# Performance work log

Hardware: AMD Instinct MI355X
Metric: run time of the kernel (lower is better)

## Reference

```python
import jax, jax.numpy as jnp
import numpy as np

B, T, C = 64, 1024, 32   # batch, seq_len, n_embd
H, D = 4, 8              # num_heads, head_size (H*D == C)


def setup_inputs() -> dict:
    key = jax.random.key(0)
    ks = jax.random.split(key, 6)
    s = 0.02  # init scale for weights
    x = jax.random.normal(ks[0], (B, T, C), dtype=jnp.float32)
    Wq = jax.random.normal(ks[1], (H, C, D), dtype=jnp.float32) * s
    Wk = jax.random.normal(ks[2], (H, C, D), dtype=jnp.float32) * s
    Wv = jax.random.normal(ks[3], (H, C, D), dtype=jnp.float32) * s
    Wproj = jax.random.normal(ks[4], (H * D, C), dtype=jnp.float32) * s
    bproj = jnp.zeros((C,), dtype=jnp.float32)
    return {"x": x, "Wq": Wq, "Wk": Wk, "Wv": Wv, "Wproj": Wproj, "bproj": bproj}


def reference(x, Wq, Wk, Wv, Wproj, bproj):
    # All heads batched into one einsum instead of a Python loop over Head modules.
    q = jnp.einsum('btc,hcd->bhtd', x, Wq)
    k = jnp.einsum('btc,hcd->bhtd', x, Wk)
    v = jnp.einsum('btc,hcd->bhtd', x, Wv)
    scale = D ** -0.5
    att = jnp.einsum('bhtd,bhsd->bhts', q, k) * scale  # [B,H,T,T]
    causal = jnp.tril(jnp.ones((T, T), dtype=bool))
    att = jnp.where(causal, att, jnp.float32(-1e9))
    att = jax.nn.softmax(att, axis=-1)  # dropout omitted (eval mode)
    o = jnp.einsum('bhts,bhsd->bhtd', att, v)
    o = o.transpose(0, 2, 1, 3).reshape(B, T, H * D)  # concat heads on last dim
    return o @ Wproj + bproj  # final proj; output dropout omitted (eval mode)
```

## Files before the change

### kernel.cpp

```cpp
#include <hip/hip_runtime.h>
#include <math.h>

static constexpr int Bb = 64, Tt = 1024, Cc = 32, Hh = 4, Dd = 8;
static constexpr float QSCALE = 0.51006973f;

typedef _Float16 h2  __attribute__((ext_vector_type(2)));
typedef _Float16 v4h __attribute__((ext_vector_type(4)));
typedef float  f32x4 __attribute__((ext_vector_type(4)));

__device__ __forceinline__ h2 pkrtz(float a, float b) {
  return __builtin_bit_cast(h2, __builtin_amdgcn_cvt_pkrtz(a, b));
}

__device__ __forceinline__ float fdot2(h2 a, h2 b, float c) {
#if __has_builtin(__builtin_amdgcn_fdot2)
  return __builtin_amdgcn_fdot2(a, b, c, false);
#else
  return fmaf((float)a.x, (float)b.x, fmaf((float)a.y, (float)b.y, c));
#endif
}

__device__ __forceinline__ float frcp(float x) {
#if __has_builtin(__builtin_amdgcn_rcpf)
  return __builtin_amdgcn_rcpf(x);
#else
  return 1.0f / x;
#endif
}

__device__ __forceinline__ float bperm_f32(int src_lane, float v) {
  return __builtin_bit_cast(float,
      __builtin_amdgcn_ds_bpermute(src_lane << 2, __builtin_bit_cast(int, v)));
}

__device__ __forceinline__ h2 exp2h2(h2 s) {
  const h2 A3 = {(_Float16)0.05550411f, (_Float16)0.05550411f};
  const h2 A2 = {(_Float16)0.24022651f, (_Float16)0.24022651f};
  const h2 A1 = {(_Float16)0.69314718f, (_Float16)0.69314718f};
  const h2 ONE = {(_Float16)1.0f, (_Float16)1.0f};
  h2 t = A3 * s + A2;
  t = t * s + A1;
  t = t * s + ONE;
  return t;
}

union U4 { uint4 u; h2 h[4]; };
union P2 { uint2 u; h2 h[2]; v4h v; };

__device__ __forceinline__ void chain_step(const P2& ak, const v4h& bv,
                                           const P2& bq, f32x4& o) {
  const f32x4 zero4 = {0.f, 0.f, 0.f, 0.f};
  f32x4 s = __builtin_amdgcn_mfma_f32_16x16x16f16(ak.v, bq.v, zero4, 0, 0, 0);
  h2 p0 = exp2h2(pkrtz(s[0], s[1]));
  h2 p1 = exp2h2(pkrtz(s[2], s[3]));
  P2 pf; pf.h[0] = p0; pf.h[1] = p1;
  o = __builtin_amdgcn_mfma_f32_16x16x16f16(pf.v, bv, o, 0, 0, 0);
}

__device__ __forceinline__ void chain_step_masked(const P2& ak, const v4h& bv,
                                                  const P2& bq, f32x4& o,
                                                  h2 km0, h2 km1) {
  const f32x4 zero4 = {0.f, 0.f, 0.f, 0.f};
  f32x4 s = __builtin_amdgcn_mfma_f32_16x16x16f16(ak.v, bq.v, zero4, 0, 0, 0);
  h2 p0 = exp2h2(pkrtz(s[0], s[1])) * km0;
  h2 p1 = exp2h2(pkrtz(s[2], s[3])) * km1;
  P2 pf; pf.h[0] = p0; pf.h[1] = p1;
  o = __builtin_amdgcn_mfma_f32_16x16x16f16(pf.v, bv, o, 0, 0, 0);
}

__global__ void qkv_kernel(
    const float* __restrict__ x, const float* __restrict__ Wq,
    const float* __restrict__ Wk, const float* __restrict__ Wv,
    ushort* __restrict__ Qg, ushort* __restrict__ Kg, ushort* __restrict__ Vg)
{
  __shared__ h2 wT[3][Hh][Dd][17];

  const int tid = threadIdx.x;
  const int b = blockIdx.x >> 2, q = blockIdx.x & 3;
  const int t = q * 256 + (tid >> 2);
  const int h = tid & 3;

  for (int e = tid; e < 1536; e += 1024) {
    const int mat = e >> 9, r = e & 511;
    const int hh = r >> 7, d = (r >> 4) & 7, c2 = r & 15;
    const float* W = (mat == 0) ? Wq : (mat == 1) ? Wk : Wv;
    const float w0 = W[(hh * Cc + 2 * c2) * Dd + d];
    const float w1 = W[(hh * Cc + 2 * c2 + 1) * Dd + d];
    wT[mat][hh][d][c2] = pkrtz(w0, w1);
  }

  h2 xr[16];
  {
    const float4* gx = (const float4*)(x + ((long)b * Tt + t) * Cc);
#pragma unroll
    for (int i = 0; i < 8; ++i) {
      float4 v = gx[i];
      xr[2 * i]     = pkrtz(v.x, v.y);
      xr[2 * i + 1] = pkrtz(v.z, v.w);
    }
  }
  __syncthreads();

  const long bh = (long)(b * Hh + h);
#pragma unroll
  for (int mat = 0; mat < 3; ++mat) {
    float a[Dd];
#pragma unroll
    for (int d = 0; d < Dd; ++d) {
      float s = 0.f;
#pragma unroll
      for (int c2 = 0; c2 < 16; ++c2) s = fdot2(xr[c2], wT[mat][h][d][c2], s);
      a[d] = s;
    }
    if (mat == 2) {
#pragma unroll
      for (int d = 0; d < Dd; ++d)
        ((_Float16*)Vg)[bh * (Dd * Tt) + d * Tt + t] = (_Float16)a[d];
    } else {
      const float sc = (mat == 0) ? QSCALE : 1.0f;
      ushort* dst = (mat == 0) ? Qg : Kg;
      U4 uu;
#pragma unroll
      for (int i = 0; i < 4; ++i)
        uu.h[i] = pkrtz(a[2 * i] * sc, a[2 * i + 1] * sc);
      ((uint4*)(dst + (bh * Tt + t) * Dd))[0] = uu.u;
    }
  }
}

__global__ void attn_kernel(
    const ushort* __restrict__ Qg, const ushort* __restrict__ Kg,
    const ushort* __restrict__ Vg, ushort* __restrict__ og)
{
  __shared__ __align__(16) ushort ks[Tt * Dd];
  __shared__ __align__(16) ushort vs[9 * 1032];

  const int tid = threadIdx.x;
  const int bh = blockIdx.x & 255;
  const int g  = blockIdx.x >> 8;
  const int b = bh >> 2, h = bh & 3;

  const int lane = tid & 63;
  const int u  = __builtin_amdgcn_readfirstlane(tid >> 6);
  const int W  = g * 8 + u;
  const int rb0 = W, rb1 = 63 - W;
  const int n = lane & 15, quad = lane >> 4;

  const ushort* Qbh = Qg + (long)bh * (Tt * Dd);
  uint2 r0 = *(const uint2*)(Qbh + (rb0 * 16 + n) * Dd + (quad & 1) * 4);
  uint2 r1 = *(const uint2*)(Qbh + (rb1 * 16 + n) * Dd + (quad & 1) * 4);

  {
    const uint4* Ksrc = (const uint4*)(Kg + (long)bh * (Tt * Dd));
    const uint4* Vsrc = (const uint4*)(Vg + (long)bh * (Tt * Dd));
    uint4* kd = (uint4*)ks;
    uint4* vd = (uint4*)vs;
#pragma unroll
    for (int i = 0; i < 2; ++i) {
      const int idx = tid + i * 512;
      kd[idx] = Ksrc[idx];
      const int d = idx >> 7, c = idx & 127;
      vd[d * 129 + c] = Vsrc[idx];
    }
    if (tid < 128) {
      const unsigned one2 = 0x3C003C00u;
      vd[1032 + tid] = make_uint4(one2, one2, one2, one2);
    }
  }
  __syncthreads();

  const ushort* kbase = ks + n * Dd + (quad & 1) * 4;
  const int vr = (n <= 8) ? n : (n - 8);
  const ushort* vbase = vs + vr * 1032 + quad * 4;

  const h2 km0 = {(_Float16)((4 * quad + 0) <= n ? 1.f : 0.f),
                  (_Float16)((4 * quad + 1) <= n ? 1.f : 0.f)};
  const h2 km1 = {(_Float16)((4 * quad + 2) <= n ? 1.f : 0.f),
                  (_Float16)((4 * quad + 3) <= n ? 1.f : 0.f)};

  P2 bq0, bq1;
  if (quad & 2) { r0.x = 0; r0.y = 0; r1.x = 0; r1.y = 0; }
  bq0.u = r0; bq1.u = r1;

  const f32x4 zero4 = {0.f, 0.f, 0.f, 0.f};
  f32x4 o0 = zero4, o1 = zero4;

#define LOAD_AKBV                                         \
  P2 ak; ak.u = *(const uint2*)(kbase + ct * 128);        \
  const v4h bv = *(const v4h*)(vbase + ct * 16);

  int ct = 0;
#pragma unroll 2
  for (; ct < rb0; ++ct) {
    LOAD_AKBV;
    chain_step(ak, bv, bq0, o0);
    chain_step(ak, bv, bq1, o1);
  }
  {
    LOAD_AKBV;
    chain_step_masked(ak, bv, bq0, o0, km0, km1);
    chain_step(ak, bv, bq1, o1);
    ++ct;
  }
#pragma unroll 2
  for (; ct < rb1; ++ct) {
    LOAD_AKBV;
    chain_step(ak, bv, bq1, o1);
  }
  {
    LOAD_AKBV;
    chain_step_masked(ak, bv, bq1, o1, km0, km1);
  }
#undef LOAD_AKBV

  const int lsrc = (lane & 48) | 8;
#pragma unroll
  for (int r = 0; r < 4; ++r) {
    const float l0 = bperm_f32(lsrc, o0[r]);
    const float ov0 = o0[r] * frcp(l0);
    const float l1 = bperm_f32(lsrc, o1[r]);
    const float ov1 = o1[r] * frcp(l1);
    if (n < 8) {
      const int q0 = rb0 * 16 + 4 * quad + r;
      const int q1 = rb1 * 16 + 4 * quad + r;
      ((_Float16*)og)[(((long)b * Tt + q0) * Hh + h) * Dd + n] = (_Float16)ov0;
      ((_Float16*)og)[(((long)b * Tt + q1) * Hh + h) * Dd + n] = (_Float16)ov1;
    }
  }
}

__global__ __launch_bounds__(256) void proj_kernel(
    const ushort* __restrict__ o_ws, const float* __restrict__ Wp,
    const float* __restrict__ bp, float* __restrict__ out)
{
  __shared__ h2 wT[Cc][17];
  __shared__ float bps[Cc];
  const int tid = threadIdx.x;
  {
    const int c = tid & 31, hp = tid >> 5;
#pragma unroll
    for (int i = 0; i < 2; ++i) {
      const int hd2 = hp + 8 * i;
      wT[c][hd2] = pkrtz(Wp[(2 * hd2) * Cc + c], Wp[(2 * hd2 + 1) * Cc + c]);
    }
    if (tid < Cc) bps[tid] = bp[tid];
  }
  __syncthreads();

  const int bt = blockIdx.x * 64 + (tid >> 2);
  const int cq = tid & 3;
  h2 orow[16];
  {
    const uint4* op = (const uint4*)(o_ws + (long)bt * Cc);
#pragma unroll
    for (int w = 0; w < 4; ++w) {
      U4 uu; uu.u = op[w];
#pragma unroll
      for (int i = 0; i < 4; ++i) orow[w * 4 + i] = uu.h[i];
    }
  }
  float acc[8];
#pragma unroll
  for (int j = 0; j < 8; ++j) {
    const int c = cq * 8 + j;
    float a = bps[c];
#pragma unroll
    for (int hd2 = 0; hd2 < 16; ++hd2) a = fdot2(orow[hd2], wT[c][hd2], a);
    acc[j] = a;
  }
  float4* og2 = (float4*)(out + (long)bt * Cc + cq * 8);
  og2[0] = make_float4(acc[0], acc[1], acc[2], acc[3]);
  og2[1] = make_float4(acc[4], acc[5], acc[6], acc[7]);
}

extern "C" void kernel_launch(void* const* d_in, const int* in_sizes, int n_in,
                              void* d_out, int out_size, void* d_ws, size_t ws_size,
                              hipStream_t stream) {
  const float* x  = (const float*)d_in[0];
  const float* Wq = (const float*)d_in[1];
  const float* Wk = (const float*)d_in[2];
  const float* Wv = (const float*)d_in[3];
  const float* Wp = (const float*)d_in[4];
  const float* bp = (const float*)d_in[5];
  float* out = (float*)d_out;

  ushort* o_ws = (ushort*)d_ws;
  ushort* Qg = (ushort*)d_ws + 2097152;
  ushort* Kg = Qg + 2097152;
  ushort* Vg = Kg + 2097152;

  qkv_kernel<<<Bb * 4, 1024, 0, stream>>>(x, Wq, Wk, Wv, Qg, Kg, Vg);
  attn_kernel<<<Bb * Hh * 4, 512, 0, stream>>>(Qg, Kg, Vg, o_ws);
  proj_kernel<<<Bb * Tt / 64, 256, 0, stream>>>(o_ws, Wp, bp, out);
}
```

Before: 102.1 us.

## Use MFMA for QKV and output projections, store V row-major

Replaces the fdot2-based QKV and projection kernels with MFMA 16x16x16 f16 kernels, where each wave handles a 16-token tile and loads weights directly from global memory instead of staging them in shared memory. V is now written in the same [bh][t][d] layout as K, and the attention kernel transposes V into its padded shared layout during the load. The intent is to cut the ALU and LDS work of the projections. In exchange, global stores become scattered 2-byte writes, every wave reloads the weights redundantly, and the transpose scatter into LDS adds cost to the attention kernel.

```diff
diff --git a/kernel.cpp b/kernel.cpp
--- a/kernel.cpp
+++ b/kernel.cpp
@@ -10,14 +10,6 @@
 
 __device__ __forceinline__ h2 pkrtz(float a, float b) {
   return __builtin_bit_cast(h2, __builtin_amdgcn_cvt_pkrtz(a, b));
-}
-
-__device__ __forceinline__ float fdot2(h2 a, h2 b, float c) {
-#if __has_builtin(__builtin_amdgcn_fdot2)
-  return __builtin_amdgcn_fdot2(a, b, c, false);
-#else
-  return fmaf((float)a.x, (float)b.x, fmaf((float)a.y, (float)b.y, c));
-#endif
 }
 
 __device__ __forceinline__ float frcp(float x) {
@@ -68,63 +60,59 @@
   o = __builtin_amdgcn_mfma_f32_16x16x16f16(pf.v, bv, o, 0, 0, 0);
 }
 
-__global__ void qkv_kernel(
+__global__ __launch_bounds__(256) void qkv_mfma_kernel(
     const float* __restrict__ x, const float* __restrict__ Wq,
     const float* __restrict__ Wk, const float* __restrict__ Wv,
     ushort* __restrict__ Qg, ushort* __restrict__ Kg, ushort* __restrict__ Vg)
 {
-  __shared__ h2 wT[3][Hh][Dd][17];
-
   const int tid = threadIdx.x;
-  const int b = blockIdx.x >> 2, q = blockIdx.x & 3;
-  const int t = q * 256 + (tid >> 2);
-  const int h = tid & 3;
-
-  for (int e = tid; e < 1536; e += 1024) {
-    const int mat = e >> 9, r = e & 511;
-    const int hh = r >> 7, d = (r >> 4) & 7, c2 = r & 15;
-    const float* W = (mat == 0) ? Wq : (mat == 1) ? Wk : Wv;
-    const float w0 = W[(hh * Cc + 2 * c2) * Dd + d];
-    const float w1 = W[(hh * Cc + 2 * c2 + 1) * Dd + d];
-    wT[mat][hh][d][c2] = pkrtz(w0, w1);
-  }
-
-  h2 xr[16];
-  {
-    const float4* gx = (const float4*)(x + ((long)b * Tt + t) * Cc);
-#pragma unroll
-    for (int i = 0; i < 8; ++i) {
-      float4 v = gx[i];
-      xr[2 * i]     = pkrtz(v.x, v.y);
-      xr[2 * i + 1] = pkrtz(v.z, v.w);
-    }
-  }
-  __syncthreads();
-
-  const long bh = (long)(b * Hh + h);
-#pragma unroll
-  for (int mat = 0; mat < 3; ++mat) {
-    float a[Dd];
-#pragma unroll
-    for (int d = 0; d < Dd; ++d) {
-      float s = 0.f;
-#pragma unroll
-      for (int c2 = 0; c2 < 16; ++c2) s = fdot2(xr[c2], wT[mat][h][d][c2], s);
-      a[d] = s;
-    }
-    if (mat == 2) {
-#pragma unroll
-      for (int d = 0; d < Dd; ++d)
-        ((_Float16*)Vg)[bh * (Dd * Tt) + d * Tt + t] = (_Float16)a[d];
-    } else {
-      const float sc = (mat == 0) ? QSCALE : 1.0f;
-      ushort* dst = (mat == 0) ? Qg : Kg;
-      U4 uu;
-#pragma unroll
-      for (int i = 0; i < 4; ++i)
-        uu.h[i] = pkrtz(a[2 * i] * sc, a[2 * i + 1] * sc);
-      ((uint4*)(dst + (bh * Tt + t) * Dd))[0] = uu.u;
-    }
+  const int lane = tid & 63;
+  const int wv = (blockIdx.x << 2) | (tid >> 6);
+  const int b = wv >> 6, tile = wv & 63;
+  const int n = lane & 15, quad = lane >> 4;
+
+  const float* xrow = x + ((long)b * Tt + tile * 16 + n) * Cc + 4 * quad;
+  const float4 xa0 = *(const float4*)(xrow);
+  const float4 xa1 = *(const float4*)(xrow + 16);
+  P2 a0, a1;
+  a0.h[0] = pkrtz(xa0.x, xa0.y); a0.h[1] = pkrtz(xa0.z, xa0.w);
+  a1.h[0] = pkrtz(xa1.x, xa1.y); a1.h[1] = pkrtz(xa1.z, xa1.w);
+
+  const int d = n & 7;
+  P2 wb[6][2];
+#pragma unroll
+  for (int ct = 0; ct < 6; ++ct) {
+    const int mat = ct >> 1;
+    const int hh = (2 * ct + (n >> 3)) & 3;
+    const float sc = (mat == 0) ? QSCALE : 1.0f;
+    const float* Wm = ((mat == 0) ? Wq : (mat == 1) ? Wk : Wv)
+                      + (hh * Cc) * Dd + d;
+#pragma unroll
+    for (int kc = 0; kc < 2; ++kc) {
+      const int ch0 = 16 * kc + 4 * quad;
+      const float w0 = Wm[(ch0 + 0) * Dd] * sc;
+      const float w1 = Wm[(ch0 + 1) * Dd] * sc;
+      const float w2 = Wm[(ch0 + 2) * Dd] * sc;
+      const float w3 = Wm[(ch0 + 3) * Dd] * sc;
+      wb[ct][kc].h[0] = pkrtz(w0, w1);
+      wb[ct][kc].h[1] = pkrtz(w2, w3);
+    }
+  }
+
+  const int t0 = tile * 16 + 4 * quad;
+  const f32x4 zero4 = {0.f, 0.f, 0.f, 0.f};
+#pragma unroll
+  for (int ct = 0; ct < 6; ++ct) {
+    f32x4 acc = zero4;
+    acc = __builtin_amdgcn_mfma_f32_16x16x16f16(a0.v, wb[ct][0].v, acc, 0, 0, 0);
+    acc = __builtin_amdgcn_mfma_f32_16x16x16f16(a1.v, wb[ct][1].v, acc, 0, 0, 0);
+    const int mat = ct >> 1;
+    const int hh = (2 * ct + (n >> 3)) & 3;
+    ushort* dst = (mat == 0) ? Qg : (mat == 1) ? Kg : Vg;
+    _Float16* base = (_Float16*)dst + (((long)b * Hh + hh) * Tt + t0) * Dd + d;
+#pragma unroll
+    for (int r = 0; r < 4; ++r)
+      base[r * Dd] = (_Float16)acc[r];
   }
 }
 
@@ -154,17 +142,20 @@
     const uint4* Ksrc = (const uint4*)(Kg + (long)bh * (Tt * Dd));
     const uint4* Vsrc = (const uint4*)(Vg + (long)bh * (Tt * Dd));
     uint4* kd = (uint4*)ks;
-    uint4* vd = (uint4*)vs;
 #pragma unroll
     for (int i = 0; i < 2; ++i) {
       const int idx = tid + i * 512;
       kd[idx] = Ksrc[idx];
-      const int d = idx >> 7, c = idx & 127;
-      vd[d * 129 + c] = Vsrc[idx];
+      U4 uu; uu.u = Vsrc[idx];
+#pragma unroll
+      for (int w = 0; w < 4; ++w) {
+        ((_Float16*)vs)[(2 * w + 0) * 1032 + idx] = uu.h[w].x;
+        ((_Float16*)vs)[(2 * w + 1) * 1032 + idx] = uu.h[w].y;
+      }
     }
     if (tid < 128) {
       const unsigned one2 = 0x3C003C00u;
-      vd[1032 + tid] = make_uint4(one2, one2, one2, one2);
+      ((uint4*)vs)[1032 + tid] = make_uint4(one2, one2, one2, one2);
     }
   }
   __syncthreads();
@@ -229,48 +220,49 @@
   }
 }
 
-__global__ __launch_bounds__(256) void proj_kernel(
+__global__ __launch_bounds__(256) void proj_mfma_kernel(
     const ushort* __restrict__ o_ws, const float* __restrict__ Wp,
     const float* __restrict__ bp, float* __restrict__ out)
 {
-  __shared__ h2 wT[Cc][17];
-  __shared__ float bps[Cc];
   const int tid = threadIdx.x;
-  {
-    const int c = tid & 31, hp = tid >> 5;
-#pragma unroll
-    for (int i = 0; i < 2; ++i) {
-      const int hd2 = hp + 8 * i;
-      wT[c][hd2] = pkrtz(Wp[(2 * hd2) * Cc + c], Wp[(2 * hd2 + 1) * Cc + c]);
-    }
-    if (tid < Cc) bps[tid] = bp[tid];
-  }
-  __syncthreads();
-
-  const int bt = blockIdx.x * 64 + (tid >> 2);
-  const int cq = tid & 3;
-  h2 orow[16];
-  {
-    const uint4* op = (const uint4*)(o_ws + (long)bt * Cc);
-#pragma unroll
-    for (int w = 0; w < 4; ++w) {
-      U4 uu; uu.u = op[w];
-#pragma unroll
-      for (int i = 0; i < 4; ++i) orow[w * 4 + i] = uu.h[i];
-    }
-  }
-  float acc[8];
-#pragma unroll
-  for (int j = 0; j < 8; ++j) {
-    const int c = cq * 8 + j;
-    float a = bps[c];
-#pragma unroll
-    for (int hd2 = 0; hd2 < 16; ++hd2) a = fdot2(orow[hd2], wT[c][hd2], a);
-    acc[j] = a;
-  }
-  float4* og2 = (float4*)(out + (long)bt * Cc + cq * 8);
-  og2[0] = make_float4(acc[0], acc[1], acc[2], acc[3]);
-  og2[1] = make_float4(acc[4], acc[5], acc[6], acc[7]);
+  const int lane = tid & 63;
+  const int wv = (blockIdx.x << 2) | (tid >> 6);
+  const int n = lane & 15, quad = lane >> 4;
+
+  const ushort* arow = o_ws + ((long)wv * 16 + n) * Cc + 4 * quad;
+  P2 a0, a1;
+  a0.u = *(const uint2*)(arow);
+  a1.u = *(const uint2*)(arow + 16);
+
+  P2 wb[2][2];
+#pragma unroll
+  for (int ct = 0; ct < 2; ++ct) {
+    const int c = 16 * ct + n;
+#pragma unroll
+    for (int kc = 0; kc < 2; ++kc) {
+      const int ch0 = 16 * kc + 4 * quad;
+      const float w0 = Wp[(ch0 + 0) * Cc + c];
+      const float w1 = Wp[(ch0 + 1) * Cc + c];
+      const float w2 = Wp[(ch0 + 2) * Cc + c];
+      const float w3 = Wp[(ch0 + 3) * Cc + c];
+      wb[ct][kc].h[0] = pkrtz(w0, w1);
+      wb[ct][kc].h[1] = pkrtz(w2, w3);
+    }
+  }
+  const float bias0 = bp[n], bias1 = bp[16 + n];
+
+  const long t0 = (long)wv * 16 + 4 * quad;
+  const f32x4 zero4 = {0.f, 0.f, 0.f, 0.f};
+#pragma unroll
+  for (int ct = 0; ct < 2; ++ct) {
+    f32x4 acc = zero4;
+    acc = __builtin_amdgcn_mfma_f32_16x16x16f16(a0.v, wb[ct][0].v, acc, 0, 0, 0);
+    acc = __builtin_amdgcn_mfma_f32_16x16x16f16(a1.v, wb[ct][1].v, acc, 0, 0, 0);
+    const float bias = (ct == 0) ? bias0 : bias1;
+#pragma unroll
+    for (int r = 0; r < 4; ++r)
+      out[(t0 + r) * Cc + 16 * ct + n] = acc[r] + bias;
+  }
 }
 
 extern "C" void kernel_launch(void* const* d_in, const int* in_sizes, int n_in,
@@ -289,7 +281,7 @@
   ushort* Kg = Qg + 2097152;
   ushort* Vg = Kg + 2097152;
 
-  qkv_kernel<<<Bb * 4, 1024, 0, stream>>>(x, Wq, Wk, Wv, Qg, Kg, Vg);
+  qkv_mfma_kernel<<<1024, 256, 0, stream>>>(x, Wq, Wk, Wv, Qg, Kg, Vg);
   attn_kernel<<<Bb * Hh * 4, 512, 0, stream>>>(Qg, Kg, Vg, o_ws);
-  proj_kernel<<<Bb * Tt / 64, 256, 0, stream>>>(o_ws, Wp, bp, out);
-}
+  proj_mfma_kernel<<<1024, 256, 0, stream>>>(o_ws, Wp, bp, out);
+}
```

After: 100.0 us. -2.1%, faster.
